# Kernel optimization log

Measured on AMD Instinct MI355X. Metric: run time of the kernel, lower is better.

## Reference

```python
import jax, jax.numpy as jnp
import numpy as np

N_S, N_RT, N_SHP, N_EXP = 1, 11, 50, 29
TOP_K, N_OBJS = 32, 32
IOU_THR = 0.4
RESIZE = 160.0
RAD2DEG = 180.0 / np.pi


def _nms_single(boxes, scores):
    # boxes: (N,4) [y1,x1,y2,x2]; scores: (N,). Greedy class-agnostic NMS
    # replicating tf.image.combined_non_max_suppression with c=1 and zero padding.
    N = scores.shape[0]
    order = jnp.argsort(-scores)
    b = boxes[order]
    s = scores[order]
    area = (b[:, 2] - b[:, 0]) * (b[:, 3] - b[:, 1])
    yy1 = jnp.maximum(b[:, None, 0], b[None, :, 0])
    xx1 = jnp.maximum(b[:, None, 1], b[None, :, 1])
    yy2 = jnp.minimum(b[:, None, 2], b[None, :, 2])
    xx2 = jnp.minimum(b[:, None, 3], b[None, :, 3])
    inter = jnp.clip(yy2 - yy1, 0.0) * jnp.clip(xx2 - xx1, 0.0)
    union = area[:, None] + area[None, :] - inter
    iou = jax.lax.stop_gradient(inter / jnp.maximum(union, 1e-8))
    idxs = jnp.arange(N)

    def body(i, supp):
        row = (iou[i] > IOU_THR) & (idxs > i) & jnp.logical_not(supp[i])
        return supp | row

    supp = jax.lax.fori_loop(0, N, body, jnp.zeros((N,), bool))
    keep = ~supp
    rank = jnp.cumsum(keep) - 1
    valid = keep & (rank < N_OBJS)
    slot = jnp.where(valid, rank, N_OBJS)  # out-of-range -> dropped
    ob = jnp.zeros((N_OBJS, 4), b.dtype).at[slot].set(b, mode='drop')
    osc = jnp.zeros((N_OBJS,), s.dtype).at[slot].set(s, mode='drop')
    ocl = jnp.zeros((N_OBJS,), s.dtype)  # single class -> class 0
    return ob, osc, ocl


def _forward(hms, pmaps, origin_shapes, pms, u_base, shp_base, exp_base):
    B, H, W, C = hms.shape  # C == 1
    resize_ratio = origin_shapes / RESIZE  # (B,2) [ry, rx]
    # keep-local-maxima via 3x3 max pool (Base.apply_max_pool)
    pooled = jax.lax.reduce_window(hms, -np.inf, jax.lax.max,
                                   (1, 3, 3, 1), (1, 1, 1, 1), 'SAME')
    peaks = jnp.where(pooled == hms, hms, 0.0)
    flat = peaks.reshape(B, H * W)
    scores, idx = jax.lax.top_k(flat, TOP_K)  # (B,N)
    ys, xs = idx // W, idx % W
    bidx = jnp.arange(B)[:, None]
    params = pmaps[bidx, ys, xs]  # (B,N,91) gather_nd
    mask = scores > 0.5  # score gating (literal 0.5 as in source)
    params = params * pms[1] + pms[0]
    s = params[..., :N_S]
    Rt = params[..., N_S:N_S + N_RT]
    shp = params[..., N_S + N_RT:N_S + N_RT + N_SHP]
    exp = params[..., N_S + N_RT + N_SHP:]
    # 3DMM vertices: (B,N,204) -> (B,N,68,3); u_base already mean-centered
    verts = (u_base[:, 0][None, None, :]
             + jnp.einsum('vp,bnp->bnv', shp_base, shp)
             + jnp.einsum('vp,bnp->bnv', exp_base, exp))
    verts = verts.reshape(B, TOP_K, 68, 3)
    Rt = jnp.concatenate([Rt, jnp.ones((B, TOP_K, 1), Rt.dtype)], -1)
    Rt = Rt.reshape(B, TOP_K, 3, 4)
    R = Rt[..., :3]  # (B,N,3,3); t column is unused (as in source)
    lnmks = s[..., None] * jnp.einsum('bnvc,bnrc->bnvr', verts, R)  # verts @ R^T
    coors = jnp.stack([ys, xs], -1).astype(jnp.float32) * resize_ratio[:, None, :]
    coors_xy = coors[..., ::-1]
    lnmks_yx = (lnmks[..., :2] + coors_xy[:, :, None, :])[..., ::-1]  # (B,N,68,2)
    tls = lnmks_yx.min(axis=2)
    brs = lnmks_yx.max(axis=2)
    bboxes = jnp.concatenate([tls, brs, scores[..., None]], -1)  # (B,N,5)
    bboxes = jnp.where(mask[..., None], bboxes, -1.0)  # invalid slots stay -1
    nb, ns, ncl = jax.vmap(_nms_single)(bboxes[..., :4], bboxes[..., 4])
    box_results = jnp.where(nb == -1.0, jnp.inf, nb)
    box_results = jnp.where(box_results == 0.0, jnp.inf, box_results)
    out_bboxes = jnp.concatenate([box_results, ns[..., None], ncl[..., None]], -1)
    # _valid_lnmks: match NMS-kept detections back to candidates by score equality
    det_valid = jnp.all(out_bboxes != jnp.inf, axis=-1)  # (B,M)
    eq = (scores[:, :, None] == ns[:, None, :]) & det_valid[:, None, :]
    matched = eq.any(-1)  # (B,N)
    lnmks_flat = lnmks_yx.reshape(B, TOP_K, 68 * 2)
    out_lnmks = jnp.where(matched[..., None], lnmks_flat, -1.0)
    out_lnmks = out_lnmks.reshape(B, N_OBJS, 68, 2)
    yaw = jnp.arcsin(-R[..., 2, 0]) * RAD2DEG
    cy = jnp.cos(yaw)  # cosine of DEGREES value, faithful to the original code
    pitch = jnp.arctan2(R[..., 2, 1] / cy, R[..., 2, 2] / cy) * RAD2DEG
    roll = jnp.arctan2(R[..., 1, 0] / cy, R[..., 0, 0] / cy) * RAD2DEG
    pose = jnp.stack([pitch, yaw, roll], -1)  # (B,N,3)
    out_pose = jnp.where(matched[..., None], pose, -1.0)
    out_lnmks = jnp.where(out_lnmks == -1.0, jnp.inf, out_lnmks)
    out_pose = jnp.where(out_pose == -1.0, jnp.inf, out_pose)
    return out_bboxes, out_lnmks, out_pose


def setup_inputs() -> dict:
    key = jax.random.key(0)
    ks = jax.random.split(key, 5)
    B, H, W = 16, 160, 160
    hms = jax.random.uniform(ks[0], (B, H, W, 1), jnp.float32)
    pmaps = jax.random.normal(ks[1], (B, H, W, 91), jnp.float32)
    origin_shapes = jnp.full((B, 2), 640.0, jnp.float32)  # 640px originals
    mean = np.zeros(91, np.float32)
    mean[0] = 0.001  # 3DMM scale
    mean[1:12] = np.array([1, 0, 0, 0, 0, 1, 0, 0, 0, 0, 1], np.float32)  # ~identity Rt
    std = np.full(91, 0.02, np.float32)
    pms = jnp.asarray(np.stack([mean, std]))  # (2,91): row0 mean, row1 std
    u = jax.random.normal(ks[2], (68, 3), jnp.float32) * 100.0
    u = u - u.mean(axis=0, keepdims=True)  # mean-centered as in __init__
    u_base = u.reshape(204, 1)
    shp_base = jax.random.normal(ks[3], (204, 50), jnp.float32)
    exp_base = jax.random.normal(ks[4], (204, 29), jnp.float32)
    return {"hms": hms, "pmaps": pmaps, "origin_shapes": origin_shapes,
            "pms": pms, "u_base": u_base, "shp_base": shp_base,
            "exp_base": exp_base}


def reference(hms, pmaps, origin_shapes, pms, u_base, shp_base, exp_base):
    return _forward(hms, pmaps, origin_shapes, pms, u_base, shp_base, exp_base)
```

## Files before the change

kernel.cpp:

```cpp
#include <hip/hip_runtime.h>
#include <math.h>

#define HW   25600
#define WID  160
#define NPAR 91
#define TOPK 32

#define CV_OFF 0
#define CI_OFF 12800
#define TV_OFF 25600
#define TI_OFF 26112
#define BB_OFF 26624
#define PS_OFF 29184
#define LN_OFF 30720

__global__ __launch_bounds__(256) void k1_peaks(const float* __restrict__ hms,
                                                float* __restrict__ wsf,
                                                int* __restrict__ wsi)
{
  const int chunk = blockIdx.x;
  const int b     = blockIdx.y;
  const int tid   = threadIdx.x;
  const float* hb = hms + (size_t)b * HW;

  __shared__ float cv[1056];
  __shared__ int   ci[1056];
  __shared__ int   cnt;
  if (tid == 0) cnt = 0;
  __syncthreads();

  const int base = chunk << 10;
  #pragma unroll
  for (int k = 0; k < 4; ++k) {
    int lp = tid + (k << 8);
    int p  = base + lp;
    int y  = p / WID, x = p - y * WID;
    float c = hb[p];
    bool peak = true;
    #pragma unroll
    for (int dy = -1; dy <= 1; ++dy) {
      #pragma unroll
      for (int dx = -1; dx <= 1; ++dx) {
        if (dy == 0 && dx == 0) continue;
        int yy = y + dy, xx = x + dx;
        if (yy < 0 || yy >= WID || xx < 0 || xx >= WID) continue;
        if (hb[yy * WID + xx] > c) peak = false;
      }
    }
    if (peak || lp < 32) {
      int slot = atomicAdd(&cnt, 1);
      cv[slot] = peak ? c : 0.0f;
      ci[slot] = p;
    }
  }
  __syncthreads();

  const int P = cnt;
  float* outv = wsf + CV_OFF + b * 800 + chunk * 32;
  int*   outi = wsi + CI_OFF + b * 800 + chunk * 32;
  for (int j = tid; j < P; j += 256) {
    float vj = cv[j]; int ij = ci[j];
    int rank = 0;
    for (int m = 0; m < P; ++m) {
      float vm = cv[m]; int im = ci[m];
      rank += (vm > vj || (vm == vj && im < ij)) ? 1 : 0;
    }
    if (rank < TOPK) { outv[rank] = vj; outi[rank] = ij; }
  }
}

__global__ __launch_bounds__(256) void k2_topk(float* __restrict__ wsf,
                                               int* __restrict__ wsi)
{
  const int seg = blockIdx.x;
  const int b   = blockIdx.y;
  const int tid = threadIdx.x;

  __shared__ float cv[800];
  __shared__ int   ci[800];
  const float* inv = wsf + CV_OFF + b * 800;
  const int*   ini = wsi + CI_OFF + b * 800;
  for (int j = tid; j < 800; j += 256) { cv[j] = inv[j]; ci[j] = ini[j]; }
  __syncthreads();

  if (tid < 200) {
    int j = seg * 200 + tid;
    float vj = cv[j]; int ij = ci[j];
    int rank = 0;
    for (int m = 0; m < 800; ++m) {
      float vm = cv[m]; int im = ci[m];
      rank += (vm > vj || (vm == vj && im < ij)) ? 1 : 0;
    }
    if (rank < TOPK) {
      wsf[TV_OFF + b * TOPK + rank] = vj;
      wsi[TI_OFF + b * TOPK + rank] = ij;
    }
  }
}

__global__ __launch_bounds__(256) void k3_verts(const float* __restrict__ pmaps,
                                                const float* __restrict__ oshapes,
                                                const float* __restrict__ pms,
                                                const float* __restrict__ ub,
                                                const float* __restrict__ sb,
                                                const float* __restrict__ eb,
                                                float* __restrict__ wsf,
                                                const int* __restrict__ wsi)
{
  const int n   = blockIdx.x;
  const int b   = blockIdx.y;
  const int tid = threadIdx.x;

  __shared__ float s_sb[10200];
  __shared__ float s_eb[5916];
  __shared__ float s_ub[204];
  __shared__ float s_prm[NPAR];
  __shared__ float s_v[204];
  __shared__ float s_pyx[136];

  {
    const float4* s4 = (const float4*)sb;
    float4* d4 = (float4*)s_sb;
    for (int i = tid; i < 2550; i += 256) d4[i] = s4[i];
    const float4* e4 = (const float4*)eb;
    float4* de = (float4*)s_eb;
    for (int i = tid; i < 1479; i += 256) de[i] = e4[i];
    if (tid < 51) ((float4*)s_ub)[tid] = ((const float4*)ub)[tid];
  }
  const int p = wsi[TI_OFF + b * TOPK + n];
  if (tid < NPAR)
    s_prm[tid] = pmaps[((size_t)b * HW + p) * NPAR + tid] * pms[NPAR + tid] + pms[tid];
  __syncthreads();

  if (tid < 204) {
    float acc = s_ub[tid];
    const float* srow = s_sb + tid * 50;
    for (int q = 0; q < 50; ++q) acc += srow[q] * s_prm[12 + q];
    const float* erow = s_eb + tid * 29;
    for (int q = 0; q < 29; ++q) acc += erow[q] * s_prm[62 + q];
    s_v[tid] = acc;
  }
  __syncthreads();

  const int ys = p / WID, xs = p - (p / WID) * WID;
  if (tid < 68) {
    float a0 = s_v[3 * tid], a1 = s_v[3 * tid + 1], a2 = s_v[3 * tid + 2];
    float s   = s_prm[0];
    float l0 = s * (a0 * s_prm[1] + a1 * s_prm[2] + a2 * s_prm[3]);
    float l1 = s * (a0 * s_prm[5] + a1 * s_prm[6] + a2 * s_prm[7]);
    float rr0 = oshapes[2 * b]     / 160.0f;
    float rr1 = oshapes[2 * b + 1] / 160.0f;
    float py = l1 + (float)ys * rr0;
    float px = l0 + (float)xs * rr1;
    float* ln = wsf + LN_OFF + ((size_t)b * TOPK + n) * 136;
    ln[2 * tid]     = py;
    ln[2 * tid + 1] = px;
    s_pyx[2 * tid]     = py;
    s_pyx[2 * tid + 1] = px;
  }
  __syncthreads();

  if (tid < 64) {
    float py = s_pyx[2 * tid], px = s_pyx[2 * tid + 1];
    float mny = py, mxy = py, mnx = px, mxx = px;
    if (tid < 4) {
      float qy = s_pyx[128 + 2 * tid], qx = s_pyx[129 + 2 * tid];
      mny = fminf(mny, qy); mxy = fmaxf(mxy, qy);
      mnx = fminf(mnx, qx); mxx = fmaxf(mxx, qx);
    }
    #pragma unroll
    for (int off = 32; off > 0; off >>= 1) {
      mny = fminf(mny, __shfl_xor(mny, off));
      mnx = fminf(mnx, __shfl_xor(mnx, off));
      mxy = fmaxf(mxy, __shfl_xor(mxy, off));
      mxx = fmaxf(mxx, __shfl_xor(mxx, off));
    }
    if (tid == 0) {
      float sc = wsf[TV_OFF + b * TOPK + n];
      bool mask = sc > 0.5f;
      float* bb = wsf + BB_OFF + ((size_t)b * TOPK + n) * 5;
      bb[0] = mask ? mny : -1.0f;
      bb[1] = mask ? mnx : -1.0f;
      bb[2] = mask ? mxy : -1.0f;
      bb[3] = mask ? mxx : -1.0f;
      bb[4] = mask ? sc  : -1.0f;
      const float R2D = 57.29577951308232f;
      float R20 = s_prm[9], R21 = s_prm[10], R22 = s_prm[11];
      float yaw = asinf(-R20) * R2D;
      float cyw = cosf(yaw);
      float pitch = atan2f(R21 / cyw, R22 / cyw) * R2D;
      float roll  = atan2f(s_prm[5] / cyw, s_prm[1] / cyw) * R2D;
      float* ps = wsf + PS_OFF + ((size_t)b * TOPK + n) * 3;
      ps[0] = pitch; ps[1] = yaw; ps[2] = roll;
    }
  }
}

__global__ __launch_bounds__(256) void k4_nms(const float* __restrict__ wsf,
                                              float* __restrict__ out)
{
  const int b   = blockIdx.x;
  const int tid = threadIdx.x;

  __shared__ float s_bbox[TOPK][5];
  __shared__ float s_topv[TOPK];
  __shared__ float s_obox[TOPK][4];
  __shared__ float s_osc[TOPK];
  __shared__ int   s_dv[TOPK];
  __shared__ int   s_match[TOPK];

  if (tid < 160) ((float*)s_bbox)[tid] = wsf[BB_OFF + b * 160 + tid];
  if (tid < TOPK) s_topv[tid] = wsf[TV_OFF + b * TOPK + tid];
  __syncthreads();

  if (tid < 64) {
    int j = tid;
    float b0 = 0.f, b1 = 0.f, b2 = 0.f, b3 = 0.f, sc = -1e30f;
    if (j < TOPK) {
      b0 = s_bbox[j][0]; b1 = s_bbox[j][1]; b2 = s_bbox[j][2]; b3 = s_bbox[j][3];
      sc = s_bbox[j][4];
    }
    float area = (b2 - b0) * (b3 - b1);
    int supp = (j >= TOPK) ? 1 : 0;
    for (int i = 0; i < TOPK; ++i) {
      float i0 = __shfl(b0, i), i1 = __shfl(b1, i);
      float i2 = __shfl(b2, i), i3 = __shfl(b3, i);
      float ia = __shfl(area, i);
      int isup = __shfl(supp, i);
      if (!isup && j > i && j < TOPK) {
        float yy1 = fmaxf(b0, i0), xx1 = fmaxf(b1, i1);
        float yy2 = fminf(b2, i2), xx2 = fminf(b3, i3);
        float inter = fmaxf(yy2 - yy1, 0.0f) * fmaxf(xx2 - xx1, 0.0f);
        float uni = area + ia - inter;
        float iou = inter / fmaxf(uni, 1e-8f);
        if (iou > 0.4f) supp = 1;
      }
    }
    bool keep = (j < TOPK) && !supp;
    unsigned long long km = __ballot(keep);
    int rank = __popcll(km & ((1ull << j) - 1ull));
    if (j < TOPK) {
      s_obox[j][0] = 0.f; s_obox[j][1] = 0.f; s_obox[j][2] = 0.f; s_obox[j][3] = 0.f;
      s_osc[j] = 0.f;
    }
    if (keep) {
      s_obox[rank][0] = b0; s_obox[rank][1] = b1;
      s_obox[rank][2] = b2; s_obox[rank][3] = b3;
      s_osc[rank] = sc;
    }
  }
  __syncthreads();

  if (tid < TOPK) {
    int dv = 1;
    #pragma unroll
    for (int c = 0; c < 4; ++c) {
      float t = s_obox[tid][c];
      if (t == -1.0f || t == 0.0f) { t = INFINITY; dv = 0; }
      s_obox[tid][c] = t;
    }
    s_dv[tid] = dv;
  }
  __syncthreads();

  if (tid < TOPK) {
    float mysc = s_topv[tid];
    int m = 0;
    for (int sl = 0; sl < TOPK; ++sl)
      if (s_dv[sl] && s_osc[sl] == mysc) m = 1;
    s_match[tid] = m;
  }
  __syncthreads();

  {
    float* outb = out + (size_t)b * 192;
    for (int j = tid; j < 192; j += 256) {
      int sl = j / 6, c = j - 6 * sl;
      float val;
      if (c < 4)       val = s_obox[sl][c];
      else if (c == 4) val = s_osc[sl];
      else             val = 0.0f;
      outb[j] = val;
    }
    const float* lnw = wsf + LN_OFF + (size_t)b * (TOPK * 136);
    float* outl = out + 3072 + (size_t)b * 4352;
    for (int j = tid; j < 4352; j += 256) {
      int n = j / 136;
      float t = lnw[j];
      outl[j] = s_match[n] ? ((t == -1.0f) ? INFINITY : t) : INFINITY;
    }
    const float* psw = wsf + PS_OFF + (size_t)b * (TOPK * 3);
    float* outp = out + 72704 + (size_t)b * 96;
    for (int j = tid; j < 96; j += 256) {
      int n = j / 3;
      float t = psw[j];
      outp[j] = s_match[n] ? ((t == -1.0f) ? INFINITY : t) : INFINITY;
    }
  }
}

extern "C" void kernel_launch(void* const* d_in, const int* in_sizes, int n_in,
                              void* d_out, int out_size, void* d_ws, size_t ws_size,
                              hipStream_t stream) {
  const float* hms   = (const float*)d_in[0];
  const float* pmaps = (const float*)d_in[1];
  const float* osh   = (const float*)d_in[2];
  const float* pms   = (const float*)d_in[3];
  const float* ub    = (const float*)d_in[4];
  const float* sb    = (const float*)d_in[5];
  const float* eb    = (const float*)d_in[6];
  float* o   = (float*)d_out;
  float* wsf = (float*)d_ws;
  int*   wsi = (int*)d_ws;

  k1_peaks<<<dim3(25, 16), 256, 0, stream>>>(hms, wsf, wsi);
  k2_topk <<<dim3(4, 16),  256, 0, stream>>>(wsf, wsi);
  k3_verts<<<dim3(32, 16), 256, 0, stream>>>(pmaps, osh, pms, ub, sb, eb, wsf, wsi);
  k4_nms  <<<16,           256, 0, stream>>>(wsf, o);
}
```

Measured before the change: 249.7 us.

## Fuse vertex projection and NMS into one per-batch 1024-thread kernel

Merges the per-detection vertex kernel and the per-batch NMS kernel into a single kernel with one 1024-thread block per batch. Each 32-lane group handles one detection, and the landmarks, boxes and poses stay in shared memory instead of going through the global workspace. This removes a kernel launch and the repeated loading of the shape and expression bases into shared memory for every detection. In exchange only 16 blocks run, and each carries a large shared-memory footprint, so the GPU is far less parallel and the per-block work is heavier.

```diff
diff --git a/kernel.cpp b/kernel.cpp
--- a/kernel.cpp
+++ b/kernel.cpp
@@ -10,9 +10,6 @@
 #define CI_OFF 12800
 #define TV_OFF 25600
 #define TI_OFF 26112
-#define BB_OFF 26624
-#define PS_OFF 29184
-#define LN_OFF 30720
 
 __global__ __launch_bounds__(256) void k1_peaks(const float* __restrict__ hms,
                                                 float* __restrict__ wsf,
@@ -98,119 +95,114 @@
   }
 }
 
-__global__ __launch_bounds__(256) void k3_verts(const float* __restrict__ pmaps,
+__global__ __launch_bounds__(1024) void k3_tail(const float* __restrict__ pmaps,
                                                 const float* __restrict__ oshapes,
                                                 const float* __restrict__ pms,
                                                 const float* __restrict__ ub,
                                                 const float* __restrict__ sb,
                                                 const float* __restrict__ eb,
-                                                float* __restrict__ wsf,
-                                                const int* __restrict__ wsi)
+                                                const float* __restrict__ wsf,
+                                                const int* __restrict__ wsi,
+                                                float* __restrict__ out)
 {
-  const int n   = blockIdx.x;
-  const int b   = blockIdx.y;
+  const int b   = blockIdx.x;
   const int tid = threadIdx.x;
 
   __shared__ float s_sb[10200];
   __shared__ float s_eb[5916];
   __shared__ float s_ub[204];
-  __shared__ float s_prm[NPAR];
-  __shared__ float s_v[204];
-  __shared__ float s_pyx[136];
+  __shared__ float s_prm[TOPK][NPAR];
+  __shared__ float s_lnm[TOPK * 136];
+  __shared__ float s_bbox[TOPK][5];
+  __shared__ float s_pose[TOPK][3];
+  __shared__ float s_topv[TOPK];
+  __shared__ int   s_ti[TOPK];
+  __shared__ float s_obox[TOPK][4];
+  __shared__ float s_osc[TOPK];
+  __shared__ int   s_dv[TOPK];
+  __shared__ int   s_match[TOPK];
 
   {
     const float4* s4 = (const float4*)sb;
     float4* d4 = (float4*)s_sb;
-    for (int i = tid; i < 2550; i += 256) d4[i] = s4[i];
+    for (int i = tid; i < 2550; i += 1024) d4[i] = s4[i];
     const float4* e4 = (const float4*)eb;
     float4* de = (float4*)s_eb;
-    for (int i = tid; i < 1479; i += 256) de[i] = e4[i];
+    for (int i = tid; i < 1479; i += 1024) de[i] = e4[i];
     if (tid < 51) ((float4*)s_ub)[tid] = ((const float4*)ub)[tid];
   }
-  const int p = wsi[TI_OFF + b * TOPK + n];
-  if (tid < NPAR)
-    s_prm[tid] = pmaps[((size_t)b * HW + p) * NPAR + tid] * pms[NPAR + tid] + pms[tid];
-  __syncthreads();
-
-  if (tid < 204) {
-    float acc = s_ub[tid];
-    const float* srow = s_sb + tid * 50;
-    for (int q = 0; q < 50; ++q) acc += srow[q] * s_prm[12 + q];
-    const float* erow = s_eb + tid * 29;
-    for (int q = 0; q < 29; ++q) acc += erow[q] * s_prm[62 + q];
-    s_v[tid] = acc;
-  }
-  __syncthreads();
-
-  const int ys = p / WID, xs = p - (p / WID) * WID;
-  if (tid < 68) {
-    float a0 = s_v[3 * tid], a1 = s_v[3 * tid + 1], a2 = s_v[3 * tid + 2];
-    float s   = s_prm[0];
-    float l0 = s * (a0 * s_prm[1] + a1 * s_prm[2] + a2 * s_prm[3]);
-    float l1 = s * (a0 * s_prm[5] + a1 * s_prm[6] + a2 * s_prm[7]);
+  if (tid < TOPK) {
+    s_topv[tid] = wsf[TV_OFF + b * TOPK + tid];
+    s_ti[tid]   = wsi[TI_OFF + b * TOPK + tid];
+  }
+  __syncthreads();
+
+  for (int j = tid; j < TOPK * NPAR; j += 1024) {
+    int n = j / NPAR, q = j - n * NPAR;
+    int p = s_ti[n];
+    s_prm[n][q] = pmaps[((size_t)b * HW + p) * NPAR + q] * pms[NPAR + q] + pms[q];
+  }
+  __syncthreads();
+
+  {
+    const int n = tid >> 5, l = tid & 31;
+    const float* prm = s_prm[n];
+    float s   = prm[0];
+    float R00 = prm[1], R01 = prm[2],  R02 = prm[3];
+    float R10 = prm[5], R11 = prm[6],  R12 = prm[7];
+    int p  = s_ti[n];
+    int ys = p / WID, xs = p - ys * WID;
     float rr0 = oshapes[2 * b]     / 160.0f;
     float rr1 = oshapes[2 * b + 1] / 160.0f;
-    float py = l1 + (float)ys * rr0;
-    float px = l0 + (float)xs * rr1;
-    float* ln = wsf + LN_OFF + ((size_t)b * TOPK + n) * 136;
-    ln[2 * tid]     = py;
-    ln[2 * tid + 1] = px;
-    s_pyx[2 * tid]     = py;
-    s_pyx[2 * tid + 1] = px;
-  }
-  __syncthreads();
-
-  if (tid < 64) {
-    float py = s_pyx[2 * tid], px = s_pyx[2 * tid + 1];
-    float mny = py, mxy = py, mnx = px, mxx = px;
-    if (tid < 4) {
-      float qy = s_pyx[128 + 2 * tid], qx = s_pyx[129 + 2 * tid];
-      mny = fminf(mny, qy); mxy = fmaxf(mxy, qy);
-      mnx = fminf(mnx, qx); mxx = fmaxf(mxx, qx);
+    float coy = (float)ys * rr0;
+    float cox = (float)xs * rr1;
+
+    float mny = INFINITY, mnx = INFINITY, mxy = -INFINITY, mxx = -INFINITY;
+    for (int vv = l; vv < 68; vv += 32) {
+      float a0 = s_ub[3 * vv], a1 = s_ub[3 * vv + 1], a2 = s_ub[3 * vv + 2];
+      const float* sr = s_sb + 3 * vv * 50;
+      for (int q = 0; q < 50; ++q) {
+        float w = prm[12 + q];
+        a0 += sr[q] * w; a1 += sr[50 + q] * w; a2 += sr[100 + q] * w;
+      }
+      const float* er = s_eb + 3 * vv * 29;
+      for (int q = 0; q < 29; ++q) {
+        float w = prm[62 + q];
+        a0 += er[q] * w; a1 += er[29 + q] * w; a2 += er[58 + q] * w;
+      }
+      float l0 = s * (a0 * R00 + a1 * R01 + a2 * R02);
+      float l1 = s * (a0 * R10 + a1 * R11 + a2 * R12);
+      float py = l1 + coy;
+      float px = l0 + cox;
+      s_lnm[n * 136 + vv * 2]     = py;
+      s_lnm[n * 136 + vv * 2 + 1] = px;
+      mny = fminf(mny, py); mnx = fminf(mnx, px);
+      mxy = fmaxf(mxy, py); mxx = fmaxf(mxx, px);
     }
     #pragma unroll
-    for (int off = 32; off > 0; off >>= 1) {
+    for (int off = 16; off > 0; off >>= 1) {
       mny = fminf(mny, __shfl_xor(mny, off));
       mnx = fminf(mnx, __shfl_xor(mnx, off));
       mxy = fmaxf(mxy, __shfl_xor(mxy, off));
       mxx = fmaxf(mxx, __shfl_xor(mxx, off));
     }
-    if (tid == 0) {
-      float sc = wsf[TV_OFF + b * TOPK + n];
+    if (l == 0) {
+      float sc = s_topv[n];
       bool mask = sc > 0.5f;
-      float* bb = wsf + BB_OFF + ((size_t)b * TOPK + n) * 5;
-      bb[0] = mask ? mny : -1.0f;
-      bb[1] = mask ? mnx : -1.0f;
-      bb[2] = mask ? mxy : -1.0f;
-      bb[3] = mask ? mxx : -1.0f;
-      bb[4] = mask ? sc  : -1.0f;
+      s_bbox[n][0] = mask ? mny : -1.0f;
+      s_bbox[n][1] = mask ? mnx : -1.0f;
+      s_bbox[n][2] = mask ? mxy : -1.0f;
+      s_bbox[n][3] = mask ? mxx : -1.0f;
+      s_bbox[n][4] = mask ? sc  : -1.0f;
+      float R20 = prm[9], R21 = prm[10], R22 = prm[11];
       const float R2D = 57.29577951308232f;
-      float R20 = s_prm[9], R21 = s_prm[10], R22 = s_prm[11];
       float yaw = asinf(-R20) * R2D;
       float cyw = cosf(yaw);
       float pitch = atan2f(R21 / cyw, R22 / cyw) * R2D;
-      float roll  = atan2f(s_prm[5] / cyw, s_prm[1] / cyw) * R2D;
-      float* ps = wsf + PS_OFF + ((size_t)b * TOPK + n) * 3;
-      ps[0] = pitch; ps[1] = yaw; ps[2] = roll;
-    }
-  }
-}
-
-__global__ __launch_bounds__(256) void k4_nms(const float* __restrict__ wsf,
-                                              float* __restrict__ out)
-{
-  const int b   = blockIdx.x;
-  const int tid = threadIdx.x;
-
-  __shared__ float s_bbox[TOPK][5];
-  __shared__ float s_topv[TOPK];
-  __shared__ float s_obox[TOPK][4];
-  __shared__ float s_osc[TOPK];
-  __shared__ int   s_dv[TOPK];
-  __shared__ int   s_match[TOPK];
-
-  if (tid < 160) ((float*)s_bbox)[tid] = wsf[BB_OFF + b * 160 + tid];
-  if (tid < TOPK) s_topv[tid] = wsf[TV_OFF + b * TOPK + tid];
+      float roll  = atan2f(R10 / cyw, R00 / cyw) * R2D;
+      s_pose[n][0] = pitch; s_pose[n][1] = yaw; s_pose[n][2] = roll;
+    }
+  }
   __syncthreads();
 
   if (tid < 64) {
@@ -274,7 +266,7 @@
 
   {
     float* outb = out + (size_t)b * 192;
-    for (int j = tid; j < 192; j += 256) {
+    for (int j = tid; j < 192; j += 1024) {
       int sl = j / 6, c = j - 6 * sl;
       float val;
       if (c < 4)       val = s_obox[sl][c];
@@ -282,18 +274,16 @@
       else             val = 0.0f;
       outb[j] = val;
     }
-    const float* lnw = wsf + LN_OFF + (size_t)b * (TOPK * 136);
     float* outl = out + 3072 + (size_t)b * 4352;
-    for (int j = tid; j < 4352; j += 256) {
+    for (int j = tid; j < 4352; j += 1024) {
       int n = j / 136;
-      float t = lnw[j];
+      float t = s_lnm[j];
       outl[j] = s_match[n] ? ((t == -1.0f) ? INFINITY : t) : INFINITY;
     }
-    const float* psw = wsf + PS_OFF + (size_t)b * (TOPK * 3);
     float* outp = out + 72704 + (size_t)b * 96;
-    for (int j = tid; j < 96; j += 256) {
+    for (int j = tid; j < 96; j += 1024) {
       int n = j / 3;
-      float t = psw[j];
+      float t = s_pose[n][j - 3 * n];
       outp[j] = s_match[n] ? ((t == -1.0f) ? INFINITY : t) : INFINITY;
     }
   }
@@ -315,6 +305,5 @@
 
   k1_peaks<<<dim3(25, 16), 256, 0, stream>>>(hms, wsf, wsi);
   k2_topk <<<dim3(4, 16),  256, 0, stream>>>(wsf, wsi);
-  k3_verts<<<dim3(32, 16), 256, 0, stream>>>(pmaps, osh, pms, ub, sb, eb, wsf, wsi);
-  k4_nms  <<<16,           256, 0, stream>>>(wsf, o);
+  k3_tail <<<16, 1024, 0, stream>>>(pmaps, osh, pms, ub, sb, eb, wsf, wsi, o);
 }
```

Result: slower. 327.3 us (+31.1%).
